# Optimization experiments

Hardware: AMD Instinct MI355X
Metric: run time of the kernel (lower is better)

Reference implementation:

```python
import jax, jax.numpy as jnp
import numpy as np

B, S, HID, NH, HD, E, K = 8, 1024, 1024, 16, 64, 8, 2
IDIM = 2 * HD  # expert internal dim
EPS = 1e-5


def layer_norm(x, g, b):
    m = jnp.mean(x, axis=-1, keepdims=True)
    v = jnp.mean(jnp.square(x - m), axis=-1, keepdims=True)
    return (x - m) * jax.lax.rsqrt(v + EPS) * g + b


def setup_inputs() -> dict:
    key = jax.random.key(0)
    ks = jax.random.split(key, 12)
    n = jax.random.normal
    return {
        "queries": n(ks[0], (B, S, HID), jnp.float32),
        "keys": n(ks[1], (B, S, HID), jnp.float32),
        "values": n(ks[2], (B, S, HID), jnp.float32),
        "memorys": n(ks[3], (B, NH, S, HD), jnp.float32),
        "Wq": n(ks[4], (HD, HD), jnp.float32) * 0.02,
        "Wk": n(ks[5], (HD, HD), jnp.float32) * 0.02,
        "Wv": n(ks[6], (HD, HD), jnp.float32) * 0.02,
        "forget_gate": n(ks[7], (HD,), jnp.float32),
        "gate_W": n(ks[8], (E, HD), jnp.float32) * 0.02,
        "gate_b": jnp.zeros((E,), jnp.float32),
        "ln1_g": jnp.ones((E, HD), jnp.float32),
        "ln1_b": jnp.zeros((E, HD), jnp.float32),
        "W1": n(ks[9], (E, IDIM, HD), jnp.float32) * 0.02,
        "ln2_g": jnp.ones((E, IDIM), jnp.float32),
        "ln2_b": jnp.zeros((E, IDIM), jnp.float32),
        "W2": n(ks[10], (E, HD, IDIM), jnp.float32) * 0.02,
        "b2": jnp.zeros((E, HD), jnp.float32),
    }


def reference(queries, keys, values, memorys, Wq, Wk, Wv, forget_gate,
              gate_W, gate_b, ln1_g, ln1_b, W1, ln2_g, ln2_b, W2, b2):
    bsz, seq, _ = queries.shape
    gelu = lambda x: jax.nn.gelu(x, approximate=False)

    # head split: [B,S,HID] -> [B,NH,S,HD]
    q = queries.reshape(bsz, seq, NH, HD).transpose(0, 2, 1, 3)
    k = keys.reshape(bsz, seq, NH, HD).transpose(0, 2, 1, 3)
    v = values.reshape(bsz, seq, NH, HD).transpose(0, 2, 1, 3)

    q_ = q @ Wq.T
    k_ = k @ Wk.T
    v_ = v @ Wv.T

    # gated memory cell
    cell = k_ * v_ + forget_gate * memorys
    current_memorys = (1.0 - forget_gate) * cell + forget_gate * memorys
    cell_values = q_ * current_memorys  # [B,NH,S,HD]

    # token-mixing MoE (per-token, over last dim)
    x = cell_values.reshape(-1, HD)  # [N, HD], N = B*NH*S
    logits = x @ gate_W.T + gate_b  # [N, E]
    topv, topi = jax.lax.top_k(logits, K)  # [N, K]
    # sparse combine weights [N, E] (raw gate values, as in the original)
    w = jnp.sum(jax.nn.one_hot(topi, E, dtype=x.dtype) * topv[..., None], axis=1)

    def expert_fwd(g1, b1, w1, g2, b2_, w2, bias2):
        h = gelu(layer_norm(x, g1, b1)) @ w1.T      # [N, IDIM]
        h = gelu(layer_norm(h, g2, b2_)) @ w2.T + bias2  # [N, HD]
        return h

    all_out = jax.vmap(expert_fwd)(ln1_g, ln1_b, W1, ln2_g, ln2_b, W2, b2)  # [E,N,HD]
    moe = jnp.einsum('ne,end->nd', w, all_out)  # [N, HD]

    token_mixing = moe.reshape(bsz, NH, seq, HD).transpose(0, 2, 1, 3).reshape(bsz, seq, NH * HD)
    return token_mixing, current_memorys
```

## Files before the change

kernel.cpp:

```cpp
#include <hip/hip_runtime.h>
#include <stdint.h>

typedef unsigned short u16;
typedef unsigned int   u32;
typedef unsigned long long u64;
typedef __attribute__((ext_vector_type(8))) short short8;
typedef __attribute__((ext_vector_type(4))) short s16x4;
typedef __attribute__((ext_vector_type(4))) float f32x4;

#define B_    8
#define S_    1024
#define HID_  1024
#define NH_   16
#define HD_   64
#define E_    8
#define IDIM_ 128
#define NTOK  (B_*NH_*S_)

#define CSTRIDE 16
#define XROW 65

__device__ __forceinline__ float bf2f(u16 u){ return __uint_as_float(((u32)u) << 16); }
__device__ __forceinline__ u16 f2bf(float f){
    u32 u = __float_as_uint(f);
    u32 r = u + 0x7fffu + ((u >> 16) & 1u);
    return (u16)(r >> 16);
}
__device__ __forceinline__ short8 frag8(const float* __restrict__ p){
    float4 a = *(const float4*)p;
    float4 b = *(const float4*)(p + 4);
    short8 r;
    r[0]=(short)f2bf(a.x); r[1]=(short)f2bf(a.y); r[2]=(short)f2bf(a.z); r[3]=(short)f2bf(a.w);
    r[4]=(short)f2bf(b.x); r[5]=(short)f2bf(b.y); r[6]=(short)f2bf(b.z); r[7]=(short)f2bf(b.w);
    return r;
}
__device__ __forceinline__ float gelu_exact(float x){
    return 0.5f * x * (1.0f + erff(x * 0.70710678118654752f));
}
__device__ __forceinline__ float gelu_f(float x){
    float z = 1.5957691216057308f * (x + 0.044715f * x * x * x);
    float e = __expf(z);
    float t = 1.0f - 2.0f / (e + 1.0f);
    return 0.5f * x * (1.0f + t);
}

__global__ void k_zero(u32* c){
    c[threadIdx.x] = 0;
}

__global__ __launch_bounds__(256) void k_prep(
    const float* __restrict__ W1, const float* __restrict__ W2,
    u16* __restrict__ wB1, u16* __restrict__ wB2, u32* __restrict__ counters)
{
    const int i = blockIdx.x*256 + threadIdx.x;
    if (blockIdx.x == 0) counters[threadIdx.x] = 0;
    wB1[i] = f2bf(W1[i]);
    wB2[i] = f2bf(W2[i]);
}

__global__ __launch_bounds__(256,4) void k_proj(
    const float* __restrict__ qin, const float* __restrict__ kin, const float* __restrict__ vin,
    const float* __restrict__ mem,
    const float* __restrict__ Wq, const float* __restrict__ Wk, const float* __restrict__ Wv,
    const float* __restrict__ fg,
    float* __restrict__ cur_out, float* __restrict__ out0)
{
    const int lane = threadIdx.x & 63;
    const int wid  = threadIdx.x >> 6;
    const int m    = lane & 15;
    const int kg   = lane >> 4;

    const int slab  = blockIdx.x;
    const int chunk = slab & 7, h = (slab >> 3) & 15, b = slab >> 7;
    const int tw    = chunk*128 + wid*32;

    const float* kbase = kin + ((size_t)b*S_)*HID_ + h*64;
    const float* vbase = vin + ((size_t)b*S_)*HID_ + h*64;
    const float* qbase = qin + ((size_t)b*S_)*HID_ + h*64;

    f32x4 accK[2][4], accV[2][4];
    const f32x4 z = {0.f,0.f,0.f,0.f};
    #pragma unroll
    for (int i=0;i<2;i++){ accK[i][0]=z;accK[i][1]=z;accK[i][2]=z;accK[i][3]=z;
                           accV[i][0]=z;accV[i][1]=z;accV[i][2]=z;accV[i][3]=z; }

    #pragma unroll
    for (int kk=0; kk<2; kk++){
        const int k0 = kk*32 + kg*8;
        short8 aF[2], bF[4];
        #pragma unroll
        for (int mt=0; mt<2; mt++) aF[mt] = frag8(kbase + (size_t)(tw + mt*16 + m)*HID_ + k0);
        #pragma unroll
        for (int ct=0; ct<4; ct++) bF[ct] = frag8(Wk + (ct*16 + m)*64 + k0);
        #pragma unroll
        for (int mt=0; mt<2; mt++)
            #pragma unroll
            for (int ct=0; ct<4; ct++)
                accK[mt][ct] = __builtin_amdgcn_mfma_f32_16x16x32_bf16(aF[mt], bF[ct], accK[mt][ct], 0,0,0);
    }
    #pragma unroll
    for (int kk=0; kk<2; kk++){
        const int k0 = kk*32 + kg*8;
        short8 aF[2], bF[4];
        #pragma unroll
        for (int mt=0; mt<2; mt++) aF[mt] = frag8(vbase + (size_t)(tw + mt*16 + m)*HID_ + k0);
        #pragma unroll
        for (int ct=0; ct<4; ct++) bF[ct] = frag8(Wv + (ct*16 + m)*64 + k0);
        #pragma unroll
        for (int mt=0; mt<2; mt++)
            #pragma unroll
            for (int ct=0; ct<4; ct++)
                accV[mt][ct] = __builtin_amdgcn_mfma_f32_16x16x32_bf16(aF[mt], bF[ct], accV[mt][ct], 0,0,0);
    }

    const size_t nb = ((size_t)(b*NH_ + h)) << 10;
    float fgv[4];
    #pragma unroll
    for (int ct=0; ct<4; ct++) fgv[ct] = fg[ct*16 + m];

    #pragma unroll
    for (int mt=0; mt<2; mt++){
        #pragma unroll
        for (int r=0; r<4; r++){
            const int tok = tw + mt*16 + kg*4 + r;
            const size_t rowo = (nb + (size_t)tok)*64;
            #pragma unroll
            for (int ct=0; ct<4; ct++){
                const int d = ct*16 + m;
                const float kd = accK[mt][ct][r];
                const float vd = accV[mt][ct][r];
                const float f  = fgv[ct];
                const float mv = mem[rowo + d];
                const float cell = kd*vd + f*mv;
                const float cur  = (1.0f - f)*cell + f*mv;
                accK[mt][ct][r] = cur;
                cur_out[rowo + d] = cur;
            }
        }
    }

    f32x4 accQ[2][4];
    #pragma unroll
    for (int i=0;i<2;i++){ accQ[i][0]=z;accQ[i][1]=z;accQ[i][2]=z;accQ[i][3]=z; }

    #pragma unroll
    for (int kk=0; kk<2; kk++){
        const int k0 = kk*32 + kg*8;
        short8 aF[2], bF[4];
        #pragma unroll
        for (int mt=0; mt<2; mt++) aF[mt] = frag8(qbase + (size_t)(tw + mt*16 + m)*HID_ + k0);
        #pragma unroll
        for (int ct=0; ct<4; ct++) bF[ct] = frag8(Wq + (ct*16 + m)*64 + k0);
        #pragma unroll
        for (int mt=0; mt<2; mt++)
            #pragma unroll
            for (int ct=0; ct<4; ct++)
                accQ[mt][ct] = __builtin_amdgcn_mfma_f32_16x16x32_bf16(aF[mt], bF[ct], accQ[mt][ct], 0,0,0);
    }

    #pragma unroll
    for (int mt=0; mt<2; mt++){
        #pragma unroll
        for (int r=0; r<4; r++){
            const int tok = tw + mt*16 + kg*4 + r;
            const size_t po = ((size_t)(b*S_ + tok)*NH_ + h)*64;
            #pragma unroll
            for (int ct=0; ct<4; ct++){
                const int d = ct*16 + m;
                out0[po + d] = accQ[mt][ct][r] * accK[mt][ct][r];
            }
        }
    }
}

__global__ __launch_bounds__(256,2) void k_gate(
    float* __restrict__ x_io, const float* __restrict__ gW, const float* __restrict__ gB,
    const float* __restrict__ l1g, const float* __restrict__ l1b,
    uint4* __restrict__ topiv, u32* __restrict__ counts, int writeXg)
{
    __shared__ float sX[256*XROW];
    __shared__ float sGW[512], sGB[8];
    __shared__ float sG1[8*XROW], sB1g[8*XROW];
    __shared__ u32 sWc[4][8];

    const int tid = threadIdx.x;
    for (int i = tid; i < 512; i += 256){
        sGW[i] = gW[i];
        const int e = i >> 6, d = i & 63;
        sG1[e*XROW+d] = l1g[i]; sB1g[e*XROW+d] = l1b[i];
    }
    if (tid < 8) sGB[tid] = gB[tid];

    const int rowBase = blockIdx.x * 256;
    const float* gsrc = x_io + ((size_t)rowBase << 6);
    #pragma unroll
    for (int j = 0; j < 16; j++){
        const int idx = j*256 + tid;
        const int row = idx >> 4, dc = idx & 15;
        float4 v = ((const float4*)gsrc)[idx];
        float* p = &sX[row*XROW + dc*4];
        p[0]=v.x; p[1]=v.y; p[2]=v.z; p[3]=v.w;
    }
    __syncthreads();

    const int pos = rowBase + tid;
    const int h  = pos & (NH_-1);
    const int bs = pos >> 4;
    const int s  = bs & (S_-1), b = bs >> 10;
    const int n  = ((b*NH_ + h) << 10) + s;

    float rx[64];
    {
        const float* xr = &sX[tid*XROW];
        #pragma unroll
        for (int d = 0; d < 64; d++) rx[d] = xr[d];
    }

    float lg[8];
    #pragma unroll
    for (int e = 0; e < 8; e++) lg[e] = sGB[e];
    float s0 = 0.f, s1 = 0.f;
    #pragma unroll
    for (int d = 0; d < 64; d++){
        const float xv = rx[d];
        s0 += xv; s1 += xv*xv;
        #pragma unroll
        for (int e = 0; e < 8; e++) lg[e] += sGW[e*64 + d] * xv;
    }

    int i1 = 0; float v1 = lg[0];
    #pragma unroll
    for (int e = 1; e < 8; e++){ if (lg[e] > v1){ v1 = lg[e]; i1 = e; } }
    int i2 = -1; float v2 = -3.0e38f;
    #pragma unroll
    for (int e = 0; e < 8; e++){ if (e != i1 && lg[e] > v2){ v2 = lg[e]; i2 = e; } }

    topiv[n] = make_uint4((u32)i1, (u32)i2, __float_as_uint(v1), __float_as_uint(v2));

    {
        const int lane = tid & 63;
        const int w    = tid >> 6;
        #pragma unroll
        for (int e = 0; e < 8; e++){
            u64 m1 = __ballot(i1 == e);
            u64 m2 = __ballot(i2 == e);
            if (lane == 0) sWc[w][e] = (u32)(__popcll(m1) + __popcll(m2));
        }
    }

    if (writeXg){
        const float mu = s0 * (1.0f/64.0f);
        const float rs = rsqrtf(s1 * (1.0f/64.0f) - mu*mu + 1e-5f);
        u32* xw = (u32*)&sX[tid*XROW];
        #pragma unroll
        for (int half = 0; half < 2; half++){
            const int ee = half ? i2 : i1;
            const float* g1 = &sG1[ee*XROW];
            const float* b1 = &sB1g[ee*XROW];
            #pragma unroll
            for (int dp = 0; dp < 32; dp++){
                const float v0 = gelu_f((rx[2*dp+0] - mu)*rs*g1[2*dp+0] + b1[2*dp+0]);
                const float vb = gelu_f((rx[2*dp+1] - mu)*rs*g1[2*dp+1] + b1[2*dp+1]);
                xw[half*32 + dp] = (u32)f2bf(v0) | ((u32)f2bf(vb) << 16);
            }
        }
    }
    __syncthreads();

    if (tid < 8){
        u32 t = sWc[0][tid] + sWc[1][tid] + sWc[2][tid] + sWc[3][tid];
        if (t) atomicAdd(&counts[tid*CSTRIDE], t);
    }

    if (writeXg){
        u16* gdst = (u16*)x_io + ((size_t)rowBase << 7);
        #pragma unroll
        for (int j = 0; j < 16; j++){
            const int idx = j*256 + tid;
            const int row = idx >> 4, dc = idx & 15;
            const u32* p = (const u32*)&sX[row*XROW] + dc*4;
            uint4 v;
            v.x = p[0]; v.y = p[1]; v.z = p[2]; v.w = p[3];
            ((uint4*)gdst)[idx] = v;
        }
    }
}

__global__ __launch_bounds__(256,2) void k_scatter(
    const uint4* __restrict__ topiv, const u32* __restrict__ counts, u32* __restrict__ cursors,
    u32* __restrict__ bucket, int2* __restrict__ slots)
{
    __shared__ u32 sC1[4][8], sC2[4][8];
    __shared__ u32 sB1[4][8], sB2w[4][8];

    const int tid = threadIdx.x;
    const int n = blockIdx.x*256 + tid;
    uint4 t = topiv[n];
    const int i1 = (int)t.x, i2 = (int)t.y;

    int off[8]; int acc = 0;
    #pragma unroll
    for (int e = 0; e < 8; e++){ off[e] = acc; acc += (int)counts[e*CSTRIDE]; }

    const int s = n & (S_-1), h = (n >> 10) & (NH_-1), b = n >> 14;
    const u32 pos32 = (u32)((b*S_ + s)*NH_ + h);

    const int lane = tid & 63;
    const int w    = tid >> 6;
    const u64 low = (1ull << lane) - 1ull;

    u64 myM1 = 0, myM2 = 0;
    #pragma unroll
    for (int e = 0; e < 8; e++){
        u64 m1 = __ballot(i1 == e);
        u64 m2 = __ballot(i2 == e);
        if (i1 == e) myM1 = m1;
        if (i2 == e) myM2 = m2;
        if (lane == 0){ sC1[w][e] = (u32)__popcll(m1); sC2[w][e] = (u32)__popcll(m2); }
    }
    __syncthreads();

    if (tid < 8){
        const int e = tid;
        u32 tot = 0;
        #pragma unroll
        for (int ww = 0; ww < 4; ww++) tot += sC1[ww][e] + sC2[ww][e];
        u32 base = tot ? atomicAdd(&cursors[e*CSTRIDE], tot) : 0;
        u32 run = base;
        #pragma unroll
        for (int ww = 0; ww < 4; ww++){
            sB1[ww][e] = run; run += sC1[ww][e];
            sB2w[ww][e] = run; run += sC2[ww][e];
        }
    }
    __syncthreads();

    const int slot1 = off[i1] + (int)sB1[w][i1] + (int)__popcll(myM1 & low);
    const int slot2 = off[i2] + (int)sB2w[w][i2] + (int)__popcll(myM2 & low);

    bucket[slot1] = (pos32 << 1);
    bucket[slot2] = (pos32 << 1) | 1u;
    slots[n] = make_int2(slot1, slot2);
}

__global__ __launch_bounds__(256,4) void k_expert_mfma(
    const float* __restrict__ x_src, const u32* __restrict__ bucket, const u32* __restrict__ counts,
    const u16* __restrict__ wB1, const u16* __restrict__ wB2,
    const float* __restrict__ l2g, const float* __restrict__ l2b,
    const float* __restrict__ b2,  u16* __restrict__ aout)
{
    const int e = blockIdx.x >> 10;
    const int c = blockIdx.x & 1023;
    const int cnt = (int)counts[e*CSTRIDE];
    const int aBase = c * 128;
    if (aBase >= cnt) return;

    int off = 0;
    #pragma unroll
    for (int ee = 0; ee < 8; ee++){ if (ee < e) off += (int)counts[ee*CSTRIDE]; }

    __shared__ __align__(16) u16 sH[4][32*128];
    __shared__ float sL2g[128], sL2b[128], sB2[64];

    const int tid = threadIdx.x;
    if (tid < 128){ sL2g[tid] = l2g[e*128+tid]; sL2b[tid] = l2b[e*128+tid]; }
    else if (tid < 192){ sB2[tid-128] = b2[e*64 + tid-128]; }
    __syncthreads();

    const int lane = tid & 63;
    const int w    = tid >> 6;
    const int m    = lane & 15;
    const int kg   = lane >> 4;
    const int tb   = aBase + w*32;
    char* sHw = (char*)(&sH[w][0]);

    const u16* xg = (const u16*)x_src;
    short8 aF[2][2];
    #pragma unroll
    for (int t = 0; t < 2; t++){
        int a = tb + t*16 + m; if (a > cnt-1) a = cnt-1;
        const u32 bv = bucket[off + a];
        const u16* rp = xg + (((size_t)(bv >> 1)) << 7) + (bv & 1u)*64;
        aF[t][0] = *(const short8*)(rp + kg*8);
        aF[t][1] = *(const short8*)(rp + 32 + kg*8);
    }

    const f32x4 z = {0.f,0.f,0.f,0.f};
    f32x4 acc1[2][8];
    #pragma unroll
    for (int t = 0; t < 2; t++)
        #pragma unroll
        for (int ct = 0; ct < 8; ct++) acc1[t][ct] = z;

    const u16* wB1e = wB1 + e*8192;
    #pragma unroll
    for (int kk = 0; kk < 2; kk++){
        const int k0 = kk*32 + kg*8;
        short8 bF[8];
        #pragma unroll
        for (int ct = 0; ct < 8; ct++)
            bF[ct] = *(const short8*)(wB1e + (ct*16 + m)*64 + k0);
        #pragma unroll
        for (int t = 0; t < 2; t++)
            #pragma unroll
            for (int ct = 0; ct < 8; ct++)
                acc1[t][ct] = __builtin_amdgcn_mfma_f32_16x16x32_bf16(aF[t][kk], bF[ct], acc1[t][ct], 0,0,0);
    }

    #pragma unroll
    for (int t = 0; t < 2; t++){
        #pragma unroll
        for (int r = 0; r < 4; r++){
            float p0 = 0.f, p1 = 0.f;
            #pragma unroll
            for (int ct = 0; ct < 8; ct++){ float v = acc1[t][ct][r]; p0 += v; p1 += v*v; }
            #pragma unroll
            for (int msk = 1; msk < 16; msk <<= 1){
                p0 += __shfl_xor(p0, msk);
                p1 += __shfl_xor(p1, msk);
            }
            const float mu = p0 * (1.0f/128.0f);
            const float rs = rsqrtf(p1 * (1.0f/128.0f) - mu*mu + 1e-5f);
            const int row = t*16 + kg*4 + r;
            #pragma unroll
            for (int ct = 0; ct < 8; ct++){
                const int col = ct*16 + m;
                *(u16*)(sHw + (((row<<8) + (col<<1)) ^ ((row&7)<<4)))
                    = f2bf(gelu_f((acc1[t][ct][r] - mu)*rs*sL2g[col] + sL2b[col]));
            }
        }
    }

    f32x4 acc2[2][4];
    #pragma unroll
    for (int t = 0; t < 2; t++)
        #pragma unroll
        for (int ct = 0; ct < 4; ct++) acc2[t][ct] = z;

    const u16* wB2e = wB2 + e*8192;
    #pragma unroll
    for (int kk = 0; kk < 4; kk++){
        const int k0 = kk*32 + kg*8;
        short8 aF2[2], bF2[4];
        #pragma unroll
        for (int t = 0; t < 2; t++){
            const int row = t*16 + m;
            aF2[t] = *(const short8*)(sHw + (((row<<8) + (k0<<1)) ^ ((row&7)<<4)));
        }
        #pragma unroll
        for (int ct = 0; ct < 4; ct++)
            bF2[ct] = *(const short8*)(wB2e + (ct*16 + m)*128 + k0);
        #pragma unroll
        for (int t = 0; t < 2; t++)
            #pragma unroll
            for (int ct = 0; ct < 4; ct++)
                acc2[t][ct] = __builtin_amdgcn_mfma_f32_16x16x32_bf16(aF2[t], bF2[ct], acc2[t][ct], 0,0,0);
    }

    #pragma unroll
    for (int t = 0; t < 2; t++){
        #pragma unroll
        for (int r = 0; r < 4; r++){
            const int row = t*16 + kg*4 + r;
            #pragma unroll
            for (int ct = 0; ct < 4; ct++){
                const int col = ct*16 + m;
                *(u16*)(sHw + (((row<<7) + (col<<1)) ^ ((row&7)<<4)))
                    = f2bf(acc2[t][ct][r] + sB2[col]);
            }
        }
    }

    #pragma unroll
    for (int it = 0; it < 4; it++){
        const int idx = it*64 + lane;
        const int row = idx >> 3, qq = idx & 7;
        if (tb + row < cnt){
            uint4 v = *(const uint4*)(sHw + (((row<<7) + (qq<<4)) ^ ((row&7)<<4)));
            *(uint4*)(aout + ((size_t)(off + tb + row) << 6) + qq*8) = v;
        }
    }
}

__global__ __launch_bounds__(256,2) void k_expert(
    const float* __restrict__ x_src, const u32* __restrict__ bucket, const u32* __restrict__ counts,
    const float* __restrict__ W1,  const float* __restrict__ W2,
    const float* __restrict__ l1g, const float* __restrict__ l1b,
    const float* __restrict__ l2g, const float* __restrict__ l2b,
    const float* __restrict__ b2,  u16* __restrict__ aout)
{
    const int e = blockIdx.x >> 9;
    const int c = blockIdx.x & 511;
    const int cnt = (int)counts[e*CSTRIDE];
    const int aBase = c * 256;
    if (aBase >= cnt) return;

    int off = 0;
    for (int ee = 0; ee < 8; ee++){ if (ee < e) off += (int)counts[ee*CSTRIDE]; }

    __shared__ float sW1[8192];
    __shared__ float sW2T[128*68];
    __shared__ float sL1g[64], sL1b[64], sL2g[128], sL2b[128], sB2[64];
    const int tid = threadIdx.x;
    for (int i = tid; i < 8192; i += 256){
        sW1[i] = W1[e*8192 + i];
        int d = i >> 7, j = i & 127;
        sW2T[j*68 + d] = W2[e*8192 + i];
    }
    if (tid < 64){ sL1g[tid] = l1g[e*64+tid]; sL1b[tid] = l1b[e*64+tid]; sB2[tid] = b2[e*64+tid]; }
    if (tid < 128){ sL2g[tid] = l2g[e*128+tid]; sL2b[tid] = l2b[e*128+tid]; }
    __syncthreads();

    const int a = aBase + tid;
    if (a >= cnt) return;
    const u32 pos32 = bucket[off + a] >> 1;

    float g[64];
    #pragma unroll
    for (int i = 0; i < 16; i++){
        float4 t = ((const float4*)(x_src + (size_t)pos32*64))[i];
        g[i*4+0]=t.x; g[i*4+1]=t.y; g[i*4+2]=t.z; g[i*4+3]=t.w;
    }

    float s0 = 0.f, s1 = 0.f;
    #pragma unroll
    for (int d = 0; d < 64; d++){ s0 += g[d]; s1 += g[d]*g[d]; }
    float m  = s0 * (1.0f/64.0f);
    float va = s1 * (1.0f/64.0f) - m*m;
    float rs = rsqrtf(va + 1e-5f);
    #pragma unroll
    for (int d = 0; d < 64; d++) g[d] = gelu_exact((g[d]-m)*rs*sL1g[d] + sL1b[d]);

    u32 hpk[64];
    float hs = 0.f, hs2 = 0.f;
    for (int jp = 0; jp < 64; jp++){
        float h0, h1;
        {
            float a0=0.f,a1=0.f,a2=0.f,a3=0.f;
            const float4* w4 = (const float4*)&sW1[(2*jp)*64];
            #pragma unroll
            for (int i = 0; i < 16; i++){
                float4 ww = w4[i];
                a0 += ww.x*g[i*4+0]; a1 += ww.y*g[i*4+1]; a2 += ww.z*g[i*4+2]; a3 += ww.w*g[i*4+3];
            }
            h0 = (a0+a1)+(a2+a3);
        }
        {
            float a0=0.f,a1=0.f,a2=0.f,a3=0.f;
            const float4* w4 = (const float4*)&sW1[(2*jp+1)*64];
            #pragma unroll
            for (int i = 0; i < 16; i++){
                float4 ww = w4[i];
                a0 += ww.x*g[i*4+0]; a1 += ww.y*g[i*4+1]; a2 += ww.z*g[i*4+2]; a3 += ww.w*g[i*4+3];
            }
            h1 = (a0+a1)+(a2+a3);
        }
        hs += h0 + h1; hs2 += h0*h0 + h1*h1;
        hpk[jp] = (u32)f2bf(h0) | ((u32)f2bf(h1) << 16);
    }
    float m2  = hs  * (1.0f/128.0f);
    float va2 = hs2 * (1.0f/128.0f) - m2*m2;
    float rs2 = rsqrtf(va2 + 1e-5f);

    float acc[64];
    #pragma unroll
    for (int d = 0; d < 64; d++) acc[d] = sB2[d];
    for (int j = 0; j < 128; j++){
        float hj = bf2f((u16)((j & 1) ? (hpk[j>>1] >> 16) : (hpk[j>>1] & 0xffffu)));
        float gh = gelu_exact((hj - m2)*rs2*sL2g[j] + sL2b[j]);
        const float4* w2t = (const float4*)&sW2T[j*68];
        #pragma unroll
        for (int d4 = 0; d4 < 16; d4++){
            float4 w = w2t[d4];
            acc[d4*4+0] += gh * w.x;
            acc[d4*4+1] += gh * w.y;
            acc[d4*4+2] += gh * w.z;
            acc[d4*4+3] += gh * w.w;
        }
    }

    u16* op = aout + (size_t)(off + a) * 64;
    #pragma unroll
    for (int dc = 0; dc < 8; dc++){
        uint4 o;
        o.x = (u32)f2bf(acc[dc*8+0]) | ((u32)f2bf(acc[dc*8+1]) << 16);
        o.y = (u32)f2bf(acc[dc*8+2]) | ((u32)f2bf(acc[dc*8+3]) << 16);
        o.z = (u32)f2bf(acc[dc*8+4]) | ((u32)f2bf(acc[dc*8+5]) << 16);
        o.w = (u32)f2bf(acc[dc*8+6]) | ((u32)f2bf(acc[dc*8+7]) << 16);
        ((uint4*)op)[dc] = o;
    }
}

__global__ __launch_bounds__(256,4) void k_combine(
    const u16* __restrict__ aout, const uint4* __restrict__ topiv,
    const int2* __restrict__ slots, float* __restrict__ out0)
{
    const int tid = threadIdx.x;
    const int p   = blockIdx.x*16 + (tid >> 4);
    const int cq  = tid & 15;

    const int h  = p & (NH_-1);
    const int bs = p >> 4;
    const int b  = bs >> 10, s = bs & (S_-1);
    const int n  = ((b*NH_ + h) << 10) + s;

    uint4 t = topiv[n];
    float w1 = __uint_as_float(t.z), w2 = __uint_as_float(t.w);
    int2 sl = slots[n];

    uint2 ua = *(const uint2*)(aout + (size_t)sl.x*64 + cq*4);
    uint2 ub = *(const uint2*)(aout + (size_t)sl.y*64 + cq*4);

    float4 o;
    o.x = w1*bf2f((u16)(ua.x & 0xffffu)) + w2*bf2f((u16)(ub.x & 0xffffu));
    o.y = w1*bf2f((u16)(ua.x >> 16))     + w2*bf2f((u16)(ub.x >> 16));
    o.z = w1*bf2f((u16)(ua.y & 0xffffu)) + w2*bf2f((u16)(ub.y & 0xffffu));
    o.w = w1*bf2f((u16)(ua.y >> 16))     + w2*bf2f((u16)(ub.y >> 16));
    *(float4*)(out0 + (size_t)p*64 + cq*4) = o;
}

extern "C" void kernel_launch(void* const* d_in, const int* in_sizes, int n_in,
                              void* d_out, int out_size, void* d_ws, size_t ws_size,
                              hipStream_t stream)
{
    const float* qin = (const float*)d_in[0];
    const float* kin = (const float*)d_in[1];
    const float* vin = (const float*)d_in[2];
    const float* mem = (const float*)d_in[3];
    const float* Wq  = (const float*)d_in[4];
    const float* Wk  = (const float*)d_in[5];
    const float* Wv  = (const float*)d_in[6];
    const float* fg  = (const float*)d_in[7];
    const float* gW  = (const float*)d_in[8];
    const float* gB  = (const float*)d_in[9];
    const float* l1g = (const float*)d_in[10];
    const float* l1b = (const float*)d_in[11];
    const float* W1  = (const float*)d_in[12];
    const float* l2g = (const float*)d_in[13];
    const float* l2b = (const float*)d_in[14];
    const float* W2  = (const float*)d_in[15];
    const float* b2  = (const float*)d_in[16];

    float* out0 = (float*)d_out;
    float* out1 = out0 + (size_t)NTOK * 64;

    char* ws = (char*)d_ws;
    u16*   aout   = (u16*)(ws);
    uint4* topiv  = (uint4*)(ws + (size_t)33554432);
    int2*  slots  = (int2*)(ws + (size_t)35651584);
    u32*   bucket = (u32*)(ws + (size_t)36700160);
    u32*   counts = (u32*)(ws + (size_t)37748736);
    u32*   cursors = (u32*)(ws + (size_t)37749248);
    u16*   wB1    = (u16*)(ws + (size_t)37749760);
    u16*   wB2    = (u16*)(ws + (size_t)37880832);
    const size_t WS_NEED = 38011904;

    (void)in_sizes; (void)n_in; (void)out_size;

    const bool use_mfma = (ws_size >= WS_NEED);

    if (use_mfma)
        k_prep <<<256, 256, 0, stream>>>(W1, W2, wB1, wB2, counts);
    else
        k_zero <<<1, 256, 0, stream>>>(counts);
    k_proj   <<<1024, 256, 0, stream>>>(qin, kin, vin, mem, Wq, Wk, Wv, fg, out1, out0);
    k_gate   <<<NTOK/256, 256, 0, stream>>>(out0, gW, gB, l1g, l1b, topiv, counts,
                                            use_mfma ? 1 : 0);
    k_scatter<<<NTOK/256, 256, 0, stream>>>(topiv, counts, cursors, bucket, slots);
    if (use_mfma)
        k_expert_mfma<<<E_*1024, 256, 0, stream>>>(out0, bucket, counts, wB1, wB2,
                                                   l2g, l2b, b2, aout);
    else
        k_expert <<<E_*512, 256, 0, stream>>>(out0, bucket, counts, W1, W2,
                                              l1g, l1b, l2g, l2b, b2, aout);
    k_combine<<<NTOK/16, 256, 0, stream>>>(aout, topiv, slots, out0);
}
```

Measured before the change: 335.7 us.

## Fuse gating, top-k and first LayerNorm+GELU into projection kernel

The projection kernel now handles 64 tokens per wave (512 blocks instead of 1024). It stages the cell values in shared memory and computes the gate logits, the top-2 selection, the per-expert counts and the bf16 LN1+GELU rows in place. This removes the separate k_gate launch and its fp32 round-trip of the cell values through global memory on the MFMA path. In exchange it uses more registers and about 70KB of shared memory, and launch bounds drop to 2 blocks per SM, which may reduce occupancy for the load-heavy projection.

```diff
diff --git a/kernel.cpp b/kernel.cpp
--- a/kernel.cpp
+++ b/kernel.cpp
@@ -58,42 +58,60 @@
     wB2[i] = f2bf(W2[i]);
 }
 
-__global__ __launch_bounds__(256,4) void k_proj(
+__global__ __launch_bounds__(256,2) void k_proj(
     const float* __restrict__ qin, const float* __restrict__ kin, const float* __restrict__ vin,
     const float* __restrict__ mem,
     const float* __restrict__ Wq, const float* __restrict__ Wk, const float* __restrict__ Wv,
     const float* __restrict__ fg,
-    float* __restrict__ cur_out, float* __restrict__ out0)
+    const float* __restrict__ gW, const float* __restrict__ gB,
+    const float* __restrict__ l1g, const float* __restrict__ l1b,
+    float* __restrict__ cur_out, float* __restrict__ out0,
+    uint4* __restrict__ topiv, u32* __restrict__ counts, int writeXg)
 {
-    const int lane = threadIdx.x & 63;
-    const int wid  = threadIdx.x >> 6;
+    __shared__ float sT[4][64*XROW];
+    __shared__ float sGW[512], sGB[8];
+    __shared__ float sG1[8*XROW], sB1g[8*XROW];
+    __shared__ u32 sWc1[4][8], sWc2[4][8];
+
+    const int tid  = threadIdx.x;
+    const int lane = tid & 63;
+    const int wid  = tid >> 6;
     const int m    = lane & 15;
     const int kg   = lane >> 4;
 
+    for (int i = tid; i < 512; i += 256){
+        sGW[i] = gW[i];
+        const int e = i >> 6, d = i & 63;
+        sG1[e*XROW+d] = l1g[i]; sB1g[e*XROW+d] = l1b[i];
+    }
+    if (tid < 8) sGB[tid] = gB[tid];
+
     const int slab  = blockIdx.x;
-    const int chunk = slab & 7, h = (slab >> 3) & 15, b = slab >> 7;
-    const int tw    = chunk*128 + wid*32;
+    const int chunk = slab & 3, h = (slab >> 2) & 15, b = slab >> 6;
+    const int tw    = chunk*256 + wid*64;
+
+    float* sW = &sT[wid][0];
 
     const float* kbase = kin + ((size_t)b*S_)*HID_ + h*64;
     const float* vbase = vin + ((size_t)b*S_)*HID_ + h*64;
     const float* qbase = qin + ((size_t)b*S_)*HID_ + h*64;
 
-    f32x4 accK[2][4], accV[2][4];
+    f32x4 accK[4][4], accV[4][4];
     const f32x4 z = {0.f,0.f,0.f,0.f};
     #pragma unroll
-    for (int i=0;i<2;i++){ accK[i][0]=z;accK[i][1]=z;accK[i][2]=z;accK[i][3]=z;
+    for (int i=0;i<4;i++){ accK[i][0]=z;accK[i][1]=z;accK[i][2]=z;accK[i][3]=z;
                            accV[i][0]=z;accV[i][1]=z;accV[i][2]=z;accV[i][3]=z; }
 
     #pragma unroll
     for (int kk=0; kk<2; kk++){
         const int k0 = kk*32 + kg*8;
-        short8 aF[2], bF[4];
-        #pragma unroll
-        for (int mt=0; mt<2; mt++) aF[mt] = frag8(kbase + (size_t)(tw + mt*16 + m)*HID_ + k0);
+        short8 aF[4], bF[4];
+        #pragma unroll
+        for (int mt=0; mt<4; mt++) aF[mt] = frag8(kbase + (size_t)(tw + mt*16 + m)*HID_ + k0);
         #pragma unroll
         for (int ct=0; ct<4; ct++) bF[ct] = frag8(Wk + (ct*16 + m)*64 + k0);
         #pragma unroll
-        for (int mt=0; mt<2; mt++)
+        for (int mt=0; mt<4; mt++)
             #pragma unroll
             for (int ct=0; ct<4; ct++)
                 accK[mt][ct] = __builtin_amdgcn_mfma_f32_16x16x32_bf16(aF[mt], bF[ct], accK[mt][ct], 0,0,0);
@@ -101,13 +119,13 @@
     #pragma unroll
     for (int kk=0; kk<2; kk++){
         const int k0 = kk*32 + kg*8;
-        short8 aF[2], bF[4];
-        #pragma unroll
-        for (int mt=0; mt<2; mt++) aF[mt] = frag8(vbase + (size_t)(tw + mt*16 + m)*HID_ + k0);
+        short8 aF[4], bF[4];
+        #pragma unroll
+        for (int mt=0; mt<4; mt++) aF[mt] = frag8(vbase + (size_t)(tw + mt*16 + m)*HID_ + k0);
         #pragma unroll
         for (int ct=0; ct<4; ct++) bF[ct] = frag8(Wv + (ct*16 + m)*64 + k0);
         #pragma unroll
-        for (int mt=0; mt<2; mt++)
+        for (int mt=0; mt<4; mt++)
             #pragma unroll
             for (int ct=0; ct<4; ct++)
                 accV[mt][ct] = __builtin_amdgcn_mfma_f32_16x16x32_bf16(aF[mt], bF[ct], accV[mt][ct], 0,0,0);
@@ -119,7 +137,7 @@
     for (int ct=0; ct<4; ct++) fgv[ct] = fg[ct*16 + m];
 
     #pragma unroll
-    for (int mt=0; mt<2; mt++){
+    for (int mt=0; mt<4; mt++){
         #pragma unroll
         for (int r=0; r<4; r++){
             const int tok = tw + mt*16 + kg*4 + r;
@@ -139,37 +157,128 @@
         }
     }
 
-    f32x4 accQ[2][4];
-    #pragma unroll
-    for (int i=0;i<2;i++){ accQ[i][0]=z;accQ[i][1]=z;accQ[i][2]=z;accQ[i][3]=z; }
+    f32x4 accQ[4][4];
+    #pragma unroll
+    for (int i=0;i<4;i++){ accQ[i][0]=z;accQ[i][1]=z;accQ[i][2]=z;accQ[i][3]=z; }
 
     #pragma unroll
     for (int kk=0; kk<2; kk++){
         const int k0 = kk*32 + kg*8;
-        short8 aF[2], bF[4];
-        #pragma unroll
-        for (int mt=0; mt<2; mt++) aF[mt] = frag8(qbase + (size_t)(tw + mt*16 + m)*HID_ + k0);
+        short8 aF[4], bF[4];
+        #pragma unroll
+        for (int mt=0; mt<4; mt++) aF[mt] = frag8(qbase + (size_t)(tw + mt*16 + m)*HID_ + k0);
         #pragma unroll
         for (int ct=0; ct<4; ct++) bF[ct] = frag8(Wq + (ct*16 + m)*64 + k0);
         #pragma unroll
-        for (int mt=0; mt<2; mt++)
+        for (int mt=0; mt<4; mt++)
             #pragma unroll
             for (int ct=0; ct<4; ct++)
                 accQ[mt][ct] = __builtin_amdgcn_mfma_f32_16x16x32_bf16(aF[mt], bF[ct], accQ[mt][ct], 0,0,0);
     }
 
-    #pragma unroll
-    for (int mt=0; mt<2; mt++){
+    if (!writeXg){
+        #pragma unroll
+        for (int mt=0; mt<4; mt++){
+            #pragma unroll
+            for (int r=0; r<4; r++){
+                const int tok = tw + mt*16 + kg*4 + r;
+                const size_t po = ((size_t)(b*S_ + tok)*NH_ + h)*64;
+                #pragma unroll
+                for (int ct=0; ct<4; ct++){
+                    const int d = ct*16 + m;
+                    out0[po + d] = accQ[mt][ct][r] * accK[mt][ct][r];
+                }
+            }
+        }
+        return;
+    }
+
+    __syncthreads();
+
+    #pragma unroll
+    for (int mt=0; mt<4; mt++){
         #pragma unroll
         for (int r=0; r<4; r++){
-            const int tok = tw + mt*16 + kg*4 + r;
-            const size_t po = ((size_t)(b*S_ + tok)*NH_ + h)*64;
+            const int trow = mt*16 + kg*4 + r;
             #pragma unroll
             for (int ct=0; ct<4; ct++){
                 const int d = ct*16 + m;
-                out0[po + d] = accQ[mt][ct][r] * accK[mt][ct][r];
-            }
-        }
+                sW[trow*XROW + d] = accQ[mt][ct][r] * accK[mt][ct][r];
+            }
+        }
+    }
+
+    const int tok = tw + lane;
+    const int pos = (b*S_ + tok)*NH_ + h;
+    const int n   = ((b*NH_ + h) << 10) + tok;
+    float rx[64];
+    {
+        const float* xr = &sW[lane*XROW];
+        #pragma unroll
+        for (int d = 0; d < 64; d++) rx[d] = xr[d];
+    }
+
+    float lg[8];
+    #pragma unroll
+    for (int e = 0; e < 8; e++) lg[e] = sGB[e];
+    float s0 = 0.f, s1 = 0.f;
+    #pragma unroll
+    for (int d = 0; d < 64; d++){
+        const float xv = rx[d];
+        s0 += xv; s1 += xv*xv;
+        #pragma unroll
+        for (int e = 0; e < 8; e++) lg[e] += sGW[e*64 + d] * xv;
+    }
+
+    int i1 = 0; float v1 = lg[0];
+    #pragma unroll
+    for (int e = 1; e < 8; e++){ if (lg[e] > v1){ v1 = lg[e]; i1 = e; } }
+    int i2 = -1; float v2 = -3.0e38f;
+    #pragma unroll
+    for (int e = 0; e < 8; e++){ if (e != i1 && lg[e] > v2){ v2 = lg[e]; i2 = e; } }
+
+    topiv[n] = make_uint4((u32)i1, (u32)i2, __float_as_uint(v1), __float_as_uint(v2));
+
+    #pragma unroll
+    for (int e = 0; e < 8; e++){
+        u64 m1 = __ballot(i1 == e);
+        u64 m2 = __ballot(i2 == e);
+        if (lane == 0){ sWc1[wid][e] = (u32)__popcll(m1); sWc2[wid][e] = (u32)__popcll(m2); }
+    }
+
+    {
+        const float mu = s0 * (1.0f/64.0f);
+        const float rs = rsqrtf(s1 * (1.0f/64.0f) - mu*mu + 1e-5f);
+        u16* xgrow = (u16*)out0 + ((size_t)pos << 7);
+        #pragma unroll
+        for (int half = 0; half < 2; half++){
+            const int ee = half ? i2 : i1;
+            const float* g1 = &sG1[ee*XROW];
+            const float* b1 = &sB1g[ee*XROW];
+            uint4* dst = (uint4*)(xgrow + half*64);
+            #pragma unroll
+            for (int dc = 0; dc < 8; dc++){
+                float vv[8];
+                #pragma unroll
+                for (int j = 0; j < 8; j++){
+                    const int d = dc*8 + j;
+                    vv[j] = gelu_f((rx[d] - mu)*rs*g1[d] + b1[d]);
+                }
+                uint4 o;
+                o.x = (u32)f2bf(vv[0]) | ((u32)f2bf(vv[1]) << 16);
+                o.y = (u32)f2bf(vv[2]) | ((u32)f2bf(vv[3]) << 16);
+                o.z = (u32)f2bf(vv[4]) | ((u32)f2bf(vv[5]) << 16);
+                o.w = (u32)f2bf(vv[6]) | ((u32)f2bf(vv[7]) << 16);
+                dst[dc] = o;
+            }
+        }
+    }
+
+    __syncthreads();
+    if (tid < 8){
+        u32 t = sWc1[0][tid] + sWc1[1][tid] + sWc1[2][tid] + sWc1[3][tid]
+              + sWc2[0][tid] + sWc2[1][tid] + sWc2[2][tid] + sWc2[3][tid];
+        if (t) atomicAdd(&counts[tid*CSTRIDE], t);
     }
 }
 
@@ -663,9 +772,11 @@
         k_prep <<<256, 256, 0, stream>>>(W1, W2, wB1, wB2, counts);
     else
         k_zero <<<1, 256, 0, stream>>>(counts);
-    k_proj   <<<1024, 256, 0, stream>>>(qin, kin, vin, mem, Wq, Wk, Wv, fg, out1, out0);
-    k_gate   <<<NTOK/256, 256, 0, stream>>>(out0, gW, gB, l1g, l1b, topiv, counts,
-                                            use_mfma ? 1 : 0);
+    k_proj   <<<512, 256, 0, stream>>>(qin, kin, vin, mem, Wq, Wk, Wv, fg,
+                                       gW, gB, l1g, l1b, out1, out0,
+                                       topiv, counts, use_mfma ? 1 : 0);
+    if (!use_mfma)
+        k_gate <<<NTOK/256, 256, 0, stream>>>(out0, gW, gB, l1g, l1b, topiv, counts, 0);
     k_scatter<<<NTOK/256, 256, 0, stream>>>(topiv, counts, cursors, bucket, slots);
     if (use_mfma)
         k_expert_mfma<<<E_*1024, 256, 0, stream>>>(out0, bucket, counts, wB1, wB2,
```

Measured after the change: 304.8 us. -9.2%, faster.
